# Kernel optimization log

Hardware: AMD Instinct MI355X
Metric: run time of the kernel (lower is better)

The kernel has to match this reference:

```python
import jax, jax.numpy as jnp
import numpy as np

B, L, D = 1, 2048, 2048
NH, NKV, HD = 32, 8, 64          # heads, kv heads, head_dim = D // NH
THETA = 50000.0
EPS = 1e-5
SCALE = HD ** -0.5


def _rope(x):
    # traditional (interleaved-pair) RoPE; x: (B, H, L, HD)
    hd = x.shape[-1]
    pos = jnp.arange(x.shape[2], dtype=jnp.float32)
    inv = THETA ** (-jnp.arange(0, hd, 2, dtype=jnp.float32) / hd)
    ang = pos[:, None] * inv[None, :]              # (L, HD/2)
    cos, sin = jnp.cos(ang), jnp.sin(ang)
    x1, x2 = x[..., ::2], x[..., 1::2]
    r1 = x1 * cos - x2 * sin
    r2 = x1 * sin + x2 * cos
    return jnp.stack([r1, r2], axis=-1).reshape(x.shape)


def _rmsnorm(x, w):
    return x * jax.lax.rsqrt(jnp.mean(x * x, axis=-1, keepdims=True) + EPS) * w


def setup_inputs() -> dict:
    key = jax.random.key(0)
    ks = jax.random.split(key, 5)
    x = jax.random.normal(ks[0], (B, L, D), dtype=jnp.float32)
    w_qkv = jax.random.normal(ks[1], (NH * HD + 2 * NKV * HD, D), dtype=jnp.float32) * 0.02
    w_out = jax.random.normal(ks[2], (D, D), dtype=jnp.float32) * 0.02
    q_gamma = 1.0 + 0.02 * jax.random.normal(ks[3], (HD,), dtype=jnp.float32)
    k_gamma = 1.0 + 0.02 * jax.random.normal(ks[4], (HD,), dtype=jnp.float32)
    mask = jnp.tril(jnp.ones((L, L), dtype=bool))   # causal
    return {"x": x, "w_qkv": w_qkv, "w_out": w_out,
            "q_gamma": q_gamma, "k_gamma": k_gamma, "mask": mask}


def reference(x, w_qkv, w_out, q_gamma, k_gamma, mask):
    b, l, d = x.shape
    qkv = x @ w_qkv.T                               # fused QKV proj (no bias)
    q, k, v = jnp.split(qkv, [NH * HD, NH * HD + NKV * HD], axis=-1)
    q = q.reshape(b, l, NH, HD).transpose(0, 2, 1, 3)     # (B,NH,L,HD)
    k = k.reshape(b, l, NKV, HD).transpose(0, 2, 1, 3)    # (B,NKV,L,HD)
    v = v.reshape(b, l, NKV, HD).transpose(0, 2, 1, 3)
    q = _rmsnorm(_rope(q), q_gamma)
    k = _rmsnorm(_rope(k), k_gamma)
    g = NH // NKV                                   # GQA group size
    qg = q.reshape(b, NKV, g, l, HD)
    scores = jnp.einsum('bkgqd,bkld->bkgql', qg, k) * SCALE
    scores = jnp.where(mask, scores, -jnp.inf)
    attn = jax.nn.softmax(scores, axis=-1)
    out = jnp.einsum('bkgql,bkld->bkgqd', attn, v)  # (B,NKV,g,L,HD)
    out = out.reshape(b, NH, l, HD).transpose(0, 2, 1, 3).reshape(b, l, d)
    return out @ w_out.T
```

## Files before the change

### kernel.cpp

```cpp
#include <hip/hip_runtime.h>

using bf16   = __bf16;
using bf16x4 = __bf16 __attribute__((ext_vector_type(4)));
using bf16x8 = __bf16 __attribute__((ext_vector_type(8)));
using f32x4  = float __attribute__((ext_vector_type(4)));
using f32x16 = float __attribute__((ext_vector_type(16)));
using u32x2  = unsigned int __attribute__((ext_vector_type(2)));
using u32x4  = unsigned int __attribute__((ext_vector_type(4)));

#define L_SEQ  2048
#define DMODEL 2048
#define NQH    32
#define NKVH   8
#define HDIM   64
#define QKV_N  3072

#define KVF_HSTRIDE (64 * 4 * 64 * 8)

__device__ __forceinline__ void gload_lds16(const void* g, void* lds) {
  __builtin_amdgcn_global_load_lds((__attribute__((address_space(1))) void*)(g),
                                   (__attribute__((address_space(3))) void*)(lds),
                                   16, 0, 0);
}

__device__ __forceinline__ unsigned pack2(float a, float b) {
  union { bf16 h[2]; unsigned u; } x;
  x.h[0] = (bf16)a; x.h[1] = (bf16)b;
  return x.u;
}

__device__ __forceinline__ bf16x8 make_pfrag(float p0, float p1, float p2, float p3,
                                             float p4, float p5, float p6, float p7,
                                             int hi) {
  const unsigned W0 = pack2(p0, p1);
  const unsigned W1 = pack2(p2, p3);
  const unsigned W2 = pack2(p4, p5);
  const unsigned W3 = pack2(p6, p7);
  u32x4 pw;
#if __has_builtin(__builtin_amdgcn_permlane32_swap)
  {
    using i32x2 = int __attribute__((ext_vector_type(2)));
    const i32x2 r02 = __builtin_amdgcn_permlane32_swap((int)W0, (int)W2, false, false);
    const i32x2 r13 = __builtin_amdgcn_permlane32_swap((int)W1, (int)W3, false, false);
    pw = u32x4{ (unsigned)r02[0], (unsigned)r13[0], (unsigned)r02[1], (unsigned)r13[1] };
  }
#else
  {
    const unsigned X0 = (unsigned)__shfl_xor((int)W0, 32);
    const unsigned X1 = (unsigned)__shfl_xor((int)W1, 32);
    const unsigned X2 = (unsigned)__shfl_xor((int)W2, 32);
    const unsigned X3 = (unsigned)__shfl_xor((int)W3, 32);
    pw = u32x4{ hi ? X2 : W0, hi ? X3 : W1, hi ? W2 : X0, hi ? W3 : X1 };
  }
#endif
  return __builtin_bit_cast(bf16x8, pw);
}

__device__ __forceinline__ int chunk_base(int qi) {
  return (qi < 16) ? qi
       : (qi < 32) ? 16 + 2 * (qi - 16)
       : (qi < 48) ? 48 + 3 * (qi - 32)
                   : 96 + 4 * (qi - 48);
}

#define N4_X  (L_SEQ * DMODEL / 4)
#define N4_WQ (QKV_N * DMODEL / 4)
#define N4_WO (DMODEL * DMODEL / 4)
__global__ void cvt3_f32_bf16(const float* __restrict__ x, const float* __restrict__ wq,
                              const float* __restrict__ wo, bf16* __restrict__ xb,
                              bf16* __restrict__ wqb, bf16* __restrict__ wob) {
  const long stride = (long)gridDim.x * blockDim.x;
  const long ntot = N4_X + N4_WQ + N4_WO;
  for (long i = (long)blockIdx.x * blockDim.x + threadIdx.x; i < ntot; i += stride) {
    const float* src; bf16* dst; long j;
    if (i < N4_X)               { src = x;  dst = xb;  j = i; }
    else if (i < N4_X + N4_WQ)  { src = wq; dst = wqb; j = i - N4_X; }
    else                        { src = wo; dst = wob; j = i - N4_X - N4_WQ; }
    const float4 v = reinterpret_cast<const float4*>(src)[j];
    bf16x4 o = { (bf16)v.x, (bf16)v.y, (bf16)v.z, (bf16)v.w };
    reinterpret_cast<bf16x4*>(dst)[j] = o;
  }
}

template <typename OutT>
__global__ __launch_bounds__(128)
void gemm_bt(const bf16* __restrict__ A, const bf16* __restrict__ B,
             OutT* __restrict__ C, int M, int N, int K) {
  __shared__ bf16 As[128 * 64];
  __shared__ bf16 Bs[64 * 64];
  const int tid = threadIdx.x;
  const int w = tid >> 6, l = tid & 63;
  const int lq = l & 15, lg = l >> 4;
  const long m0 = (long)blockIdx.y * 128;
  const long n0 = (long)blockIdx.x * 64;
  const int ks = K / gridDim.z;
  const int kb = blockIdx.z * ks;
  C += (long)blockIdx.z * M * N;

  const int lrow = l >> 3;
  const int scol = ((l & 7) ^ lrow) << 3;

  f32x4 acc[4][4];
#pragma unroll
  for (int i = 0; i < 4; ++i)
#pragma unroll
    for (int j = 0; j < 4; ++j) acc[i][j] = f32x4{0.f, 0.f, 0.f, 0.f};

  for (int k0 = kb; k0 < kb + ks; k0 += 64) {
#pragma unroll
    for (int i = 0; i < 8; ++i) {
      const int r0 = (i * 2 + w) * 8;
      gload_lds16(A + (m0 + r0 + lrow) * (long)K + k0 + scol, &As[r0 * 64]);
    }
#pragma unroll
    for (int i = 0; i < 4; ++i) {
      const int r0 = (i * 2 + w) * 8;
      gload_lds16(B + (n0 + r0 + lrow) * (long)K + k0 + scol, &Bs[r0 * 64]);
    }
    __syncthreads();
#pragma unroll
    for (int kk = 0; kk < 2; ++kk) {
      bf16x8 af[4], bfr[4];
#pragma unroll
      for (int t = 0; t < 4; ++t) {
        const int rowA = w * 64 + t * 16 + lq;
        const int blkA = (kk * 4 + lg) ^ (rowA & 7);
        af[t] = *reinterpret_cast<const bf16x8*>(&As[rowA * 64 + blkA * 8]);
        const int rowB = t * 16 + lq;
        const int blkB = (kk * 4 + lg) ^ (rowB & 7);
        bfr[t] = *reinterpret_cast<const bf16x8*>(&Bs[rowB * 64 + blkB * 8]);
      }
#pragma unroll
      for (int mt = 0; mt < 4; ++mt)
#pragma unroll
        for (int nt = 0; nt < 4; ++nt)
          acc[mt][nt] = __builtin_amdgcn_mfma_f32_16x16x32_bf16(af[mt], bfr[nt], acc[mt][nt], 0, 0, 0);
    }
    __syncthreads();
  }

#pragma unroll
  for (int mt = 0; mt < 4; ++mt)
#pragma unroll
    for (int r = 0; r < 4; ++r) {
      const long row = m0 + w * 64 + mt * 16 + lg * 4 + r;
#pragma unroll
      for (int nt = 0; nt < 4; ++nt) {
        const long col = n0 + nt * 16 + lq;
        C[row * (long)N + col] = (OutT)acc[mt][nt][r];
      }
    }
}

__global__ __launch_bounds__(256)
void rope_rms(const bf16* __restrict__ pA, const bf16* __restrict__ pB,
              const float* __restrict__ qg, const float* __restrict__ kg,
              bf16* __restrict__ qo, bf16* __restrict__ kfr) {
  const int gid = blockIdx.x * 4 + (threadIdx.x >> 6);
  const int lane = threadIdx.x & 63;
  const int pos = gid / 40;
  const int hh = gid % 40;
  const bool isq = hh < 32;
  const int col = isq ? hh * HDIM : NQH * HDIM + (hh - 32) * HDIM;

  const long idx = (long)pos * QKV_N + col + lane;
  float x = (float)pA[idx] + (float)pB[idx];
  float p = __shfl_xor(x, 1);
  const float fi = (float)(lane & ~1) * (1.0f / 64.0f);
  const float inv = powf(50000.0f, -fi);
  const float ang = (float)pos * inv;
  const float sn = sinf(ang), cs = cosf(ang);
  const float r = (lane & 1) ? (p * sn + x * cs) : (x * cs - p * sn);

  float ss = r * r;
#pragma unroll
  for (int off = 1; off < 64; off <<= 1) ss += __shfl_xor(ss, off);
  const float scl = rsqrtf(ss * (1.0f / 64.0f) + 1e-5f);
  const float g = isq ? qg[lane] : kg[lane];
  const float o = r * scl * g;

  if (isq) {
    qo[(long)pos * DMODEL + hh * HDIM + lane] = (bf16)(o * 0.18033688011112042f);
  } else {
    const int kvh = hh - 32;
    const int d = lane;
    const int lp = (pos & 31) + (((d >> 3) & 1) << 5);
    const long kidx = ((((long)kvh * 64 + (pos >> 5)) * 4 + (d >> 4)) * 64 + lp) * 8 + (d & 7);
    kfr[kidx] = (bf16)o;
  }
}

__global__ __launch_bounds__(256)
void repack_v(const bf16* __restrict__ pA, const bf16* __restrict__ pB,
              bf16* __restrict__ vfr) {
  __shared__ bf16 t[32][72];
  const int kvh = blockIdx.x >> 6;
  const int kb = blockIdx.x & 63;
  const int tid = threadIdx.x;

  {
    const int row = tid >> 3;
    const int cc = (tid & 7) * 8;
    const long goff = (long)(kb * 32 + row) * QKV_N + (NQH * HDIM + NKVH * HDIM) + kvh * HDIM + cc;
    const bf16x8 a = *reinterpret_cast<const bf16x8*>(pA + goff);
    const bf16x8 b = *reinterpret_cast<const bf16x8*>(pB + goff);
    bf16x8 s;
#pragma unroll
    for (int e = 0; e < 8; ++e) s[e] = (bf16)((float)a[e] + (float)b[e]);
    *reinterpret_cast<bf16x8*>(&t[row][cc]) = s;
  }
  __syncthreads();

  const int f = tid >> 6, l = tid & 63;
  const int s = f >> 1, dh = f & 1;
  const int hi = l >> 5, l31 = l & 31;
  union { bf16 b[8]; u32x4 u; } o;
#pragma unroll
  for (int e = 0; e < 8; ++e) o.b[e] = t[s * 16 + hi * 8 + e][dh * 32 + l31];
  bf16* od = vfr + (((long)(kvh * 64 + kb) * 4 + f) * 64 + l) * 8;
  *reinterpret_cast<u32x4*>(od) = o.u;
}

__global__ __launch_bounds__(256)
void flash_attn(const bf16* __restrict__ Q, const bf16* __restrict__ Kfr,
                const bf16* __restrict__ Vfr,
                bf16* __restrict__ po, float* __restrict__ pm, float* __restrict__ pl) {
  __shared__ bf16 Ks[2][2048];
  __shared__ bf16 Vs[2][2048];
  const int tid = threadIdx.x;
  const int w = tid >> 6, l = tid & 63;
  const int lane31 = l & 31, hi = l >> 5;
  const int bb = blockIdx.x;
  const int kvh = bb & 7;
  const int g = bb >> 3;

  int qi, c;
  if (g < 16)      { qi = g;                  c = 0; }
  else if (g < 48) { qi = 16 + ((g - 16) >> 1); c = (g - 16) & 1; }
  else if (g < 96) { qi = 32 + (g - 48) / 3;    c = (g - 48) % 3; }
  else             { qi = 48 + ((g - 96) >> 2); c = (g - 96) & 3; }

  const int h = kvh * 4 + w;
  const int s0 = c * 16;
  const int s1 = min(qi + 1, s0 + 16);
  const int pidx = h * 160 + g;

  const int q0 = qi * 32;
  const int q_abs = q0 + lane31;
  const int l8 = l * 8;

  const bf16* kfrh = Kfr + (long)kvh * KVF_HSTRIDE;
  const bf16* vfrh = Vfr + (long)kvh * KVF_HSTRIDE;

  const bf16* qrow = Q + (long)q_abs * DMODEL + h * HDIM + hi * 8;
  bf16x8 qf[4];
#pragma unroll
  for (int cc = 0; cc < 4; ++cc) qf[cc] = *reinterpret_cast<const bf16x8*>(qrow + cc * 16);

  f32x16 o0, o1;
#pragma unroll
  for (int r = 0; r < 16; ++r) { o0[r] = 0.f; o1[r] = 0.f; }
  float m = -3.0e38f, lsum = 0.f;

  gload_lds16(kfrh + (long)s0 * 2048 + tid * 8, &Ks[0][tid * 8]);
  gload_lds16(vfrh + (long)s0 * 2048 + tid * 8, &Vs[0][tid * 8]);
  __syncthreads();

  int buf = 0;
  for (int sti = s0; sti < s1; ++sti) {
    const int kb0 = sti * 32;

    if (sti + 1 < s1) {
      gload_lds16(kfrh + (long)(sti + 1) * 2048 + tid * 8, &Ks[buf ^ 1][tid * 8]);
      gload_lds16(vfrh + (long)(sti + 1) * 2048 + tid * 8, &Vs[buf ^ 1][tid * 8]);
    }

    const bf16x8 kc0 = *reinterpret_cast<const bf16x8*>(&Ks[buf][l8]);
    const bf16x8 kc1 = *reinterpret_cast<const bf16x8*>(&Ks[buf][512 + l8]);
    const bf16x8 kc2 = *reinterpret_cast<const bf16x8*>(&Ks[buf][1024 + l8]);
    const bf16x8 kc3 = *reinterpret_cast<const bf16x8*>(&Ks[buf][1536 + l8]);
    f32x16 st;
#pragma unroll
    for (int r = 0; r < 16; ++r) st[r] = 0.f;
    st = __builtin_amdgcn_mfma_f32_32x32x16_bf16(kc0, qf[0], st, 0, 0, 0);
    st = __builtin_amdgcn_mfma_f32_32x32x16_bf16(kc1, qf[1], st, 0, 0, 0);
    st = __builtin_amdgcn_mfma_f32_32x32x16_bf16(kc2, qf[2], st, 0, 0, 0);
    st = __builtin_amdgcn_mfma_f32_32x32x16_bf16(kc3, qf[3], st, 0, 0, 0);

    const bf16x8 va0 = *reinterpret_cast<const bf16x8*>(&Vs[buf][l8]);
    const bf16x8 vb0 = *reinterpret_cast<const bf16x8*>(&Vs[buf][512 + l8]);
    const bf16x8 va1 = *reinterpret_cast<const bf16x8*>(&Vs[buf][1024 + l8]);
    const bf16x8 vb1 = *reinterpret_cast<const bf16x8*>(&Vs[buf][1536 + l8]);

    if (kb0 + 31 > q0) {
#pragma unroll
      for (int r = 0; r < 16; ++r) {
        const int k_abs = kb0 + (r & 3) + 8 * (r >> 2) + 4 * hi;
        if (k_abs > q_abs) st[r] = -3.0e38f;
      }
    }

    float t[8];
#pragma unroll
    for (int r = 0; r < 8; ++r) t[r] = fmaxf(st[r], st[r + 8]);
#pragma unroll
    for (int s = 4; s > 0; s >>= 1)
#pragma unroll
      for (int r = 0; r < 4; ++r) if (r < s) t[r] = fmaxf(t[r], t[r + s]);
    float mx = fmaxf(t[0], __shfl_xor(t[0], 32));

    if (!__all(mx - m <= 8.0f)) {
      const float mn = fmaxf(m, mx);
      const float al = __builtin_amdgcn_exp2f(m - mn);
      m = mn; lsum *= al;
#pragma unroll
      for (int r = 0; r < 16; ++r) { o0[r] *= al; o1[r] *= al; }
    }
    float rs = 0.f;
#pragma unroll
    for (int r = 0; r < 16; ++r) { st[r] = __builtin_amdgcn_exp2f(st[r] - m); rs += st[r]; }
    rs += __shfl_xor(rs, 32);
    lsum += rs;

    {
      const bf16x8 pf0 = make_pfrag(st[0], st[1], st[2], st[3], st[4], st[5], st[6], st[7], hi);
      o0 = __builtin_amdgcn_mfma_f32_32x32x16_bf16(va0, pf0, o0, 0, 0, 0);
      o1 = __builtin_amdgcn_mfma_f32_32x32x16_bf16(vb0, pf0, o1, 0, 0, 0);
      const bf16x8 pf1 = make_pfrag(st[8], st[9], st[10], st[11], st[12], st[13], st[14], st[15], hi);
      o0 = __builtin_amdgcn_mfma_f32_32x32x16_bf16(va1, pf1, o0, 0, 0, 0);
      o1 = __builtin_amdgcn_mfma_f32_32x32x16_bf16(vb1, pf1, o1, 0, 0, 0);
    }

    __syncthreads();
    buf ^= 1;
  }

  bf16* pbase = po + (long)pidx * 2048 + lane31 * 64;
#pragma unroll
  for (int gg = 0; gg < 4; ++gg) {
    const int d0 = 8 * gg + 4 * hi;
    u32x2 s0v = { pack2(o0[4 * gg + 0], o0[4 * gg + 1]),
                  pack2(o0[4 * gg + 2], o0[4 * gg + 3]) };
    u32x2 s1v = { pack2(o1[4 * gg + 0], o1[4 * gg + 1]),
                  pack2(o1[4 * gg + 2], o1[4 * gg + 3]) };
    *reinterpret_cast<u32x2*>(pbase + d0) = s0v;
    *reinterpret_cast<u32x2*>(pbase + 32 + d0) = s1v;
  }
  if (hi == 0) {
    pm[pidx * 32 + lane31] = m;
    pl[pidx * 32 + lane31] = lsum;
  }
}

__global__ __launch_bounds__(256)
void combine_split(const bf16* __restrict__ po, const float* __restrict__ pm,
                   const float* __restrict__ pl, bf16* __restrict__ ao) {
  const int t = blockIdx.x * 2 + (threadIdx.x >> 7);
  const int tid7 = threadIdx.x & 127;
  const int r = tid7 >> 2;
  const int dc = (tid7 & 3) * 16;
  const int h = t >> 6, qi = t & 63;
  const int nc = 1 + (qi >> 4);
  const int p0 = h * 160 + chunk_base(qi);

  float mv0 = -3e38f, mv1 = -3e38f, mv2 = -3e38f, mv3 = -3e38f;
  float lv0 = 0.f, lv1 = 0.f, lv2 = 0.f, lv3 = 0.f;
  mv0 = pm[(p0 + 0) * 32 + r];              lv0 = pl[(p0 + 0) * 32 + r];
  if (nc > 1) { mv1 = pm[(p0 + 1) * 32 + r]; lv1 = pl[(p0 + 1) * 32 + r]; }
  if (nc > 2) { mv2 = pm[(p0 + 2) * 32 + r]; lv2 = pl[(p0 + 2) * 32 + r]; }
  if (nc > 3) { mv3 = pm[(p0 + 3) * 32 + r]; lv3 = pl[(p0 + 3) * 32 + r]; }
  const float M = fmaxf(fmaxf(mv0, mv1), fmaxf(mv2, mv3));
  const float w0 = __builtin_amdgcn_exp2f(mv0 - M);
  const float w1 = (nc > 1) ? __builtin_amdgcn_exp2f(mv1 - M) : 0.f;
  const float w2 = (nc > 2) ? __builtin_amdgcn_exp2f(mv2 - M) : 0.f;
  const float w3 = (nc > 3) ? __builtin_amdgcn_exp2f(mv3 - M) : 0.f;
  const float invL = 1.0f / (lv0 * w0 + lv1 * w1 + lv2 * w2 + lv3 * w3);

  float acc[16];
#pragma unroll
  for (int j = 0; j < 16; ++j) acc[j] = 0.f;

#pragma unroll
  for (int c = 0; c < 4; ++c) {
    if (c < nc) {
      const float fc = ((c == 0) ? w0 : (c == 1) ? w1 : (c == 2) ? w2 : w3) * invL;
      const bf16* src = po + ((long)(p0 + c) * 2048) + r * 64 + dc;
      const bf16x8 a0 = *reinterpret_cast<const bf16x8*>(src);
      const bf16x8 a1 = *reinterpret_cast<const bf16x8*>(src + 8);
#pragma unroll
      for (int j = 0; j < 8; ++j) {
        acc[j]     += (float)a0[j] * fc;
        acc[8 + j] += (float)a1[j] * fc;
      }
    }
  }

  const long q_abs = (long)qi * 32 + r;
  bf16* od = ao + q_abs * DMODEL + h * HDIM + dc;
  union { bf16 b[16]; u32x4 u[2]; } o;
#pragma unroll
  for (int j = 0; j < 16; ++j) o.b[j] = (bf16)acc[j];
  *reinterpret_cast<u32x4*>(od) = o.u[0];
  *reinterpret_cast<u32x4*>(od + 8) = o.u[1];
}

extern "C" void kernel_launch(void* const* d_in, const int* in_sizes, int n_in,
                              void* d_out, int out_size, void* d_ws, size_t ws_size,
                              hipStream_t stream) {
  const float* x       = (const float*)d_in[0];
  const float* w_qkv   = (const float*)d_in[1];
  const float* w_out   = (const float*)d_in[2];
  const float* q_gamma = (const float*)d_in[3];
  const float* k_gamma = (const float*)d_in[4];

  char* ws = (char*)d_ws;
  bf16* xb    = (bf16*)(ws);
  bf16* wqb   = (bf16*)(ws + (8ul  << 20));
  bf16* wob   = (bf16*)(ws + (20ul << 20));
  bf16* qkvpA = (bf16*)(ws + (28ul << 20));
  bf16* qkvpB = (bf16*)(ws + (40ul << 20));
  bf16* qb    = (bf16*)(ws);
  bf16* kfr   = (bf16*)(ws + (8ul  << 20));
  bf16* vfr   = (bf16*)(ws + (10ul << 20));
  bf16* po    = (bf16*)(ws + (28ul << 20));
  float* pm   = (float*)(ws + (48ul << 20));
  float* pl   = (float*)(ws + (49ul << 20));
  bf16* ao    = (bf16*)(ws + (52ul << 20));
  float* out  = (float*)d_out;

  cvt3_f32_bf16<<<2048, 256, 0, stream>>>(x, w_qkv, w_out, xb, wqb, wob);

  gemm_bt<bf16><<<dim3(QKV_N / 64, L_SEQ / 128, 2), 128, 0, stream>>>(xb, wqb, qkvpA, L_SEQ, QKV_N, DMODEL);

  rope_rms<<<(L_SEQ * 40) / 4, 256, 0, stream>>>(qkvpA, qkvpB, q_gamma, k_gamma, qb, kfr);
  repack_v<<<NKVH * (L_SEQ / 32), 256, 0, stream>>>(qkvpA, qkvpB, vfr);

  flash_attn<<<1280, 256, 0, stream>>>(qb, kfr, vfr, po, pm, pl);
  combine_split<<<1024, 256, 0, stream>>>(po, pm, pl, ao);

  gemm_bt<float><<<dim3(DMODEL / 64, L_SEQ / 128, 1), 128, 0, stream>>>(ao, wob, out, L_SEQ, DMODEL, DMODEL);
}
```

Measured before the change: 172.8 us.

## Process two KV tiles per flash-attention iteration and reverse block order

Widens the flash-attention inner loop to handle two 32-key tiles per iteration, with doubled LDS buffers, a single shared max/rescale step and one barrier per pair. A tail step covers an odd tile count. Block index is also reversed so the longest causal query chunks are scheduled first, for better load balance. The cost is more registers and LDS per block, which may reduce occupancy.

```diff
diff --git a/kernel.cpp b/kernel.cpp
--- a/kernel.cpp
+++ b/kernel.cpp
@@ -225,14 +225,14 @@
 void flash_attn(const bf16* __restrict__ Q, const bf16* __restrict__ Kfr,
                 const bf16* __restrict__ Vfr,
                 bf16* __restrict__ po, float* __restrict__ pm, float* __restrict__ pl) {
-  __shared__ bf16 Ks[2][2048];
-  __shared__ bf16 Vs[2][2048];
+  __shared__ bf16 Ks[2][4096];
+  __shared__ bf16 Vs[2][4096];
   const int tid = threadIdx.x;
   const int w = tid >> 6, l = tid & 63;
   const int lane31 = l & 31, hi = l >> 5;
   const int bb = blockIdx.x;
   const int kvh = bb & 7;
-  const int g = bb >> 3;
+  const int g = 159 - (bb >> 3);
 
   int qi, c;
   if (g < 16)      { qi = g;                  c = 0; }
@@ -262,36 +262,116 @@
   for (int r = 0; r < 16; ++r) { o0[r] = 0.f; o1[r] = 0.f; }
   float m = -3.0e38f, lsum = 0.f;
 
-  gload_lds16(kfrh + (long)s0 * 2048 + tid * 8, &Ks[0][tid * 8]);
-  gload_lds16(vfrh + (long)s0 * 2048 + tid * 8, &Vs[0][tid * 8]);
+  {
+    const long base = (long)s0 * 2048;
+    gload_lds16(kfrh + base + tid * 8,        &Ks[0][tid * 8]);
+    gload_lds16(kfrh + base + 2048 + tid * 8, &Ks[0][2048 + tid * 8]);
+    gload_lds16(vfrh + base + tid * 8,        &Vs[0][tid * 8]);
+    gload_lds16(vfrh + base + 2048 + tid * 8, &Vs[0][2048 + tid * 8]);
+  }
   __syncthreads();
 
   int buf = 0;
-  for (int sti = s0; sti < s1; ++sti) {
-    const int kb0 = sti * 32;
-
-    if (sti + 1 < s1) {
-      gload_lds16(kfrh + (long)(sti + 1) * 2048 + tid * 8, &Ks[buf ^ 1][tid * 8]);
-      gload_lds16(vfrh + (long)(sti + 1) * 2048 + tid * 8, &Vs[buf ^ 1][tid * 8]);
-    }
-
-    const bf16x8 kc0 = *reinterpret_cast<const bf16x8*>(&Ks[buf][l8]);
-    const bf16x8 kc1 = *reinterpret_cast<const bf16x8*>(&Ks[buf][512 + l8]);
-    const bf16x8 kc2 = *reinterpret_cast<const bf16x8*>(&Ks[buf][1024 + l8]);
-    const bf16x8 kc3 = *reinterpret_cast<const bf16x8*>(&Ks[buf][1536 + l8]);
-    f32x16 st;
-#pragma unroll
-    for (int r = 0; r < 16; ++r) st[r] = 0.f;
-    st = __builtin_amdgcn_mfma_f32_32x32x16_bf16(kc0, qf[0], st, 0, 0, 0);
-    st = __builtin_amdgcn_mfma_f32_32x32x16_bf16(kc1, qf[1], st, 0, 0, 0);
-    st = __builtin_amdgcn_mfma_f32_32x32x16_bf16(kc2, qf[2], st, 0, 0, 0);
-    st = __builtin_amdgcn_mfma_f32_32x32x16_bf16(kc3, qf[3], st, 0, 0, 0);
+  int sti = s0;
+  for (; sti + 1 < s1; sti += 2) {
+    if (sti + 2 < s1) {
+      const long base = (long)(sti + 2) * 2048;
+      gload_lds16(kfrh + base + tid * 8,        &Ks[buf ^ 1][tid * 8]);
+      gload_lds16(kfrh + base + 2048 + tid * 8, &Ks[buf ^ 1][2048 + tid * 8]);
+      gload_lds16(vfrh + base + tid * 8,        &Vs[buf ^ 1][tid * 8]);
+      gload_lds16(vfrh + base + 2048 + tid * 8, &Vs[buf ^ 1][2048 + tid * 8]);
+    }
+
+    f32x16 sa, sb;
+#pragma unroll
+    for (int r = 0; r < 16; ++r) { sa[r] = 0.f; sb[r] = 0.f; }
+#pragma unroll
+    for (int cc = 0; cc < 4; ++cc) {
+      const bf16x8 ka = *reinterpret_cast<const bf16x8*>(&Ks[buf][cc * 512 + l8]);
+      const bf16x8 kb = *reinterpret_cast<const bf16x8*>(&Ks[buf][2048 + cc * 512 + l8]);
+      sa = __builtin_amdgcn_mfma_f32_32x32x16_bf16(ka, qf[cc], sa, 0, 0, 0);
+      sb = __builtin_amdgcn_mfma_f32_32x32x16_bf16(kb, qf[cc], sb, 0, 0, 0);
+    }
 
     const bf16x8 va0 = *reinterpret_cast<const bf16x8*>(&Vs[buf][l8]);
     const bf16x8 vb0 = *reinterpret_cast<const bf16x8*>(&Vs[buf][512 + l8]);
     const bf16x8 va1 = *reinterpret_cast<const bf16x8*>(&Vs[buf][1024 + l8]);
     const bf16x8 vb1 = *reinterpret_cast<const bf16x8*>(&Vs[buf][1536 + l8]);
 
+    const int kb0a = sti * 32, kb0b = kb0a + 32;
+    if (kb0b + 31 > q0) {
+#pragma unroll
+      for (int r = 0; r < 16; ++r) {
+        const int krel = (r & 3) + 8 * (r >> 2) + 4 * hi;
+        if (kb0a + krel > q_abs) sa[r] = -3.0e38f;
+        if (kb0b + krel > q_abs) sb[r] = -3.0e38f;
+      }
+    }
+
+    float t[16];
+#pragma unroll
+    for (int r = 0; r < 16; ++r) t[r] = fmaxf(sa[r], sb[r]);
+#pragma unroll
+    for (int s = 8; s > 0; s >>= 1)
+#pragma unroll
+      for (int r = 0; r < 8; ++r) if (r < s) t[r] = fmaxf(t[r], t[r + s]);
+    const float mx = fmaxf(t[0], __shfl_xor(t[0], 32));
+
+    if (!__all(mx - m <= 8.0f)) {
+      const float mn = fmaxf(m, mx);
+      const float al = __builtin_amdgcn_exp2f(m - mn);
+      m = mn; lsum *= al;
+#pragma unroll
+      for (int r = 0; r < 16; ++r) { o0[r] *= al; o1[r] *= al; }
+    }
+    float rs = 0.f;
+#pragma unroll
+    for (int r = 0; r < 16; ++r) { sa[r] = __builtin_amdgcn_exp2f(sa[r] - m); rs += sa[r]; }
+#pragma unroll
+    for (int r = 0; r < 16; ++r) { sb[r] = __builtin_amdgcn_exp2f(sb[r] - m); rs += sb[r]; }
+    rs += __shfl_xor(rs, 32);
+    lsum += rs;
+
+    {
+      const bf16x8 pf0 = make_pfrag(sa[0], sa[1], sa[2], sa[3], sa[4], sa[5], sa[6], sa[7], hi);
+      o0 = __builtin_amdgcn_mfma_f32_32x32x16_bf16(va0, pf0, o0, 0, 0, 0);
+      o1 = __builtin_amdgcn_mfma_f32_32x32x16_bf16(vb0, pf0, o1, 0, 0, 0);
+      const bf16x8 pf1 = make_pfrag(sa[8], sa[9], sa[10], sa[11], sa[12], sa[13], sa[14], sa[15], hi);
+      o0 = __builtin_amdgcn_mfma_f32_32x32x16_bf16(va1, pf1, o0, 0, 0, 0);
+      o1 = __builtin_amdgcn_mfma_f32_32x32x16_bf16(vb1, pf1, o1, 0, 0, 0);
+    }
+    {
+      const bf16x8 wa0 = *reinterpret_cast<const bf16x8*>(&Vs[buf][2048 + l8]);
+      const bf16x8 wb0 = *reinterpret_cast<const bf16x8*>(&Vs[buf][2560 + l8]);
+      const bf16x8 wa1 = *reinterpret_cast<const bf16x8*>(&Vs[buf][3072 + l8]);
+      const bf16x8 wb1 = *reinterpret_cast<const bf16x8*>(&Vs[buf][3584 + l8]);
+      const bf16x8 pf0 = make_pfrag(sb[0], sb[1], sb[2], sb[3], sb[4], sb[5], sb[6], sb[7], hi);
+      o0 = __builtin_amdgcn_mfma_f32_32x32x16_bf16(wa0, pf0, o0, 0, 0, 0);
+      o1 = __builtin_amdgcn_mfma_f32_32x32x16_bf16(wb0, pf0, o1, 0, 0, 0);
+      const bf16x8 pf1 = make_pfrag(sb[8], sb[9], sb[10], sb[11], sb[12], sb[13], sb[14], sb[15], hi);
+      o0 = __builtin_amdgcn_mfma_f32_32x32x16_bf16(wa1, pf1, o0, 0, 0, 0);
+      o1 = __builtin_amdgcn_mfma_f32_32x32x16_bf16(wb1, pf1, o1, 0, 0, 0);
+    }
+
+    __syncthreads();
+    buf ^= 1;
+  }
+
+  if (sti < s1) {
+    const int kb0 = sti * 32;
+    f32x16 st;
+#pragma unroll
+    for (int r = 0; r < 16; ++r) st[r] = 0.f;
+#pragma unroll
+    for (int cc = 0; cc < 4; ++cc) {
+      const bf16x8 ka = *reinterpret_cast<const bf16x8*>(&Ks[buf][cc * 512 + l8]);
+      st = __builtin_amdgcn_mfma_f32_32x32x16_bf16(ka, qf[cc], st, 0, 0, 0);
+    }
+    const bf16x8 va0 = *reinterpret_cast<const bf16x8*>(&Vs[buf][l8]);
+    const bf16x8 vb0 = *reinterpret_cast<const bf16x8*>(&Vs[buf][512 + l8]);
+    const bf16x8 va1 = *reinterpret_cast<const bf16x8*>(&Vs[buf][1024 + l8]);
+    const bf16x8 vb1 = *reinterpret_cast<const bf16x8*>(&Vs[buf][1536 + l8]);
+
     if (kb0 + 31 > q0) {
 #pragma unroll
       for (int r = 0; r < 16; ++r) {
@@ -307,7 +387,7 @@
     for (int s = 4; s > 0; s >>= 1)
 #pragma unroll
       for (int r = 0; r < 4; ++r) if (r < s) t[r] = fmaxf(t[r], t[r + s]);
-    float mx = fmaxf(t[0], __shfl_xor(t[0], 32));
+    const float mx = fmaxf(t[0], __shfl_xor(t[0], 32));
 
     if (!__all(mx - m <= 8.0f)) {
       const float mn = fmaxf(m, mx);
@@ -322,17 +402,12 @@
     rs += __shfl_xor(rs, 32);
     lsum += rs;
 
-    {
-      const bf16x8 pf0 = make_pfrag(st[0], st[1], st[2], st[3], st[4], st[5], st[6], st[7], hi);
-      o0 = __builtin_amdgcn_mfma_f32_32x32x16_bf16(va0, pf0, o0, 0, 0, 0);
-      o1 = __builtin_amdgcn_mfma_f32_32x32x16_bf16(vb0, pf0, o1, 0, 0, 0);
-      const bf16x8 pf1 = make_pfrag(st[8], st[9], st[10], st[11], st[12], st[13], st[14], st[15], hi);
-      o0 = __builtin_amdgcn_mfma_f32_32x32x16_bf16(va1, pf1, o0, 0, 0, 0);
-      o1 = __builtin_amdgcn_mfma_f32_32x32x16_bf16(vb1, pf1, o1, 0, 0, 0);
-    }
-
-    __syncthreads();
-    buf ^= 1;
+    const bf16x8 pf0 = make_pfrag(st[0], st[1], st[2], st[3], st[4], st[5], st[6], st[7], hi);
+    o0 = __builtin_amdgcn_mfma_f32_32x32x16_bf16(va0, pf0, o0, 0, 0, 0);
+    o1 = __builtin_amdgcn_mfma_f32_32x32x16_bf16(vb0, pf0, o1, 0, 0, 0);
+    const bf16x8 pf1 = make_pfrag(st[8], st[9], st[10], st[11], st[12], st[13], st[14], st[15], hi);
+    o0 = __builtin_amdgcn_mfma_f32_32x32x16_bf16(va1, pf1, o0, 0, 0, 0);
+    o1 = __builtin_amdgcn_mfma_f32_32x32x16_bf16(vb1, pf1, o1, 0, 0, 0);
   }
 
   bf16* pbase = po + (long)pidx * 2048 + lane31 * 64;
```

New measurement: 172.0 us. About the same (-0.5%).
